# Performance work log

Hardware: AMD Instinct MI355X
Metric: run time of the kernel (lower is better)

Reference implementation:

```python
import jax, jax.numpy as jnp
import numpy as np

OMEGA_0 = 30.0  # SIREN frequency from config.kernel.omega_0


def setup_inputs() -> dict:
    key = jax.random.key(0)
    ks = jax.random.split(key, 8)
    B, Ci, Co, L, H = 8, 64, 64, 8192, 32
    x = jax.random.normal(ks[0], (B, Ci, L), dtype=jnp.float32)
    # SIREN-style kernel-net params (Linear(1,H) -> sin -> Linear(H,H) -> sin -> Linear(H, Co*Ci))
    w1 = jax.random.uniform(ks[1], (1, H), jnp.float32, -1.0, 1.0)
    b1 = jax.random.uniform(ks[2], (H,), jnp.float32, -1.0, 1.0)
    c = np.sqrt(6.0 / H) / OMEGA_0
    w2 = jax.random.uniform(ks[3], (H, H), jnp.float32, -c, c)
    b2 = jax.random.uniform(ks[4], (H,), jnp.float32, -c, c)
    w3 = jax.random.uniform(ks[5], (H, Co * Ci), jnp.float32, -c, c)
    b3 = jax.random.uniform(ks[6], (Co * Ci,), jnp.float32, -c, c)
    bias = jnp.zeros((Co,), dtype=jnp.float32)  # CKConv bias init: fill_(0.0)
    return {"x": x, "w1": w1, "b1": b1, "w2": w2, "b2": b2,
            "w3": w3, "b3": b3, "bias": bias}


def reference(x, w1, b1, w2, b2, w3, b3, bias):
    B, Ci, L = x.shape
    Co = bias.shape[0]
    # 1. relative positions in [-1, 1], one per input sample
    rel = jnp.linspace(-1.0, 1.0, L).astype(x.dtype)[:, None]        # (L, 1)
    # 2. SIREN kernel net -> continuous kernel sampled at L positions
    h = jnp.sin(OMEGA_0 * (rel @ w1 + b1))                            # (L, H)
    h = jnp.sin(OMEGA_0 * (h @ w2 + b2))                              # (L, H)
    k = (h @ w3 + b3)                                                 # (L, Co*Ci)
    kernel = k.T.reshape(Co, Ci, L)                                   # (Co, Ci, L)
    # 3. causal full-length conv1d. torch's causal_padding (left zero-pad of
    #    x by K-1, plus a left zero on an even-length kernel) + conv1d
    #    (cross-correlation) is mathematically y[t] = sum_{tau<=t} x[t-tau] *
    #    kernel_flipped[tau], i.e. a causal linear convolution with the
    #    time-reversed kernel. Computed exactly via zero-padded FFT (N=2L >=
    #    L+L-1, so no circular wraparound) instead of O(L^2) direct conv.
    kr = kernel[:, :, ::-1]                                           # flip time axis
    N = 2 * L
    Xf = jnp.fft.rfft(x, n=N, axis=-1)                                # (B, Ci, N/2+1)
    Kf = jnp.fft.rfft(kr, n=N, axis=-1)                               # (Co, Ci, N/2+1)
    Yf = jnp.einsum('bif,oif->bof', Xf, Kf)                           # contract in-channels
    y = jnp.fft.irfft(Yf, n=N, axis=-1)[:, :, :L]                     # (B, Co, L)
    return y + bias[None, :, None]
```

## Files before the change

### kernel.cpp

```cpp
#include <hip/hip_runtime.h>


#define LSEQ   8192
#define N2     8192
#define HDIM   32
#define NB     33
#define NROWS  512
#define NFREQ  8193
#define FSTRIDE 8200
#define FBLK   8
#define OMEGA0 30.0f
#define TWOPI  6.283185307179586f

#define IDX(i) ((i) + ((i) >> 4))

__global__ __launch_bounds__(256) void prep_basis_kernel(
    const float* __restrict__ w1, const float* __restrict__ b1,
    const float* __restrict__ w2, const float* __restrict__ b2,
    float* __restrict__ hbT)
{
    int t = blockIdx.x * 256 + threadIdx.x;
    float rel = -1.0f + 2.0f * (float)t / (float)(LSEQ - 1);
    float h1[HDIM];
    #pragma unroll
    for (int j = 0; j < HDIM; ++j)
        h1[j] = sinf(OMEGA0 * fmaf(rel, w1[j], b1[j]));
    for (int j = 0; j < HDIM; ++j) {
        float acc = b2[j];
        #pragma unroll 8
        for (int j2 = 0; j2 < HDIM; ++j2)
            acc = fmaf(h1[j2], w2[j2 * HDIM + j], acc);
        hbT[j * LSEQ + (LSEQ - 1 - t)] = sinf(OMEGA0 * acc);
    }
    hbT[HDIM * LSEQ + t] = 1.0f;
}

__global__ __launch_bounds__(256) void prep_m2_kernel(
    const float* __restrict__ w3, const float* __restrict__ b3,
    float* __restrict__ M2)
{
    int idx = blockIdx.x * 256 + threadIdx.x;
    if (idx >= NB * 64 * 64) return;
    int o = idx & 63;
    int i = (idx >> 6) & 63;
    int r = idx >> 12;
    M2[idx] = (r < HDIM) ? w3[r * 4096 + o * 64 + i] : b3[o * 64 + i];
}

__device__ __forceinline__ float2 tw8k(const float2* Tq, int t)
{
    bool mir = t > 1024;
    int u = mir ? 2048 - t : t;
    float2 e = Tq[u];
    float c = mir ? e.y : e.x;
    float s = mir ? e.x : e.y;
    return make_float2(c, -s);
}

__device__ __forceinline__ void build_table(float2* Tq, int tid)
{
    for (int t = tid; t <= 1024; t += 256) {
        float s, c;
        __sincosf(TWOPI * (float)t / 8192.0f, &s, &c);
        Tq[t] = make_float2(c, s);
    }
}

__device__ __forceinline__ void fft8192_core(float* re, float* im,
                                             const float2* Tq, int tid)
{
    for (int p = 11; p >= 1; p -= 2) {
        int m = 1 << p;
        int lmul = 11 - p;
        __syncthreads();
        for (int u = tid; u < 2048; u += 256) {
            int j = u & (m - 1);
            int base = ((u >> p) << (p + 2)) + j;
            int i0 = IDX(base), i1 = IDX(base + m), i2 = IDX(base + 2 * m), i3 = IDX(base + 3 * m);
            float ar = re[i0], ai = im[i0];
            float br = re[i1], bi = im[i1];
            float cr = re[i2], ci = im[i2];
            float dr = re[i3], di = im[i3];
            float t0r = ar + cr, t0i = ai + ci;
            float t1r = ar - cr, t1i = ai - ci;
            float t2r = br + dr, t2i = bi + di;
            float t3r = br - dr, t3i = bi - di;
            float q0r = t0r + t2r, q0i = t0i + t2i;
            float q2r = t0r - t2r, q2i = t0i - t2i;
            float q1r = t1r + t3i, q1i = t1i - t3r;
            float q3r = t1r - t3i, q3i = t1i + t3r;
            float2 w1 = tw8k(Tq, j << lmul);
            float w2r = w1.x * w1.x - w1.y * w1.y;
            float w2i = 2.0f * w1.x * w1.y;
            float w3r = w2r * w1.x - w2i * w1.y;
            float w3i = w2r * w1.y + w2i * w1.x;
            re[i0] = q0r;                     im[i0] = q0i;
            re[i1] = q2r * w2r - q2i * w2i;   im[i1] = q2r * w2i + q2i * w2r;
            re[i2] = q1r * w1.x - q1i * w1.y; im[i2] = q1r * w1.y + q1i * w1.x;
            re[i3] = q3r * w3r - q3i * w3i;   im[i3] = q3r * w3i + q3i * w3r;
        }
    }
    __syncthreads();
    for (int u = tid; u < 4096; u += 256) {
        int a = IDX(2 * u), b = IDX(2 * u + 1);
        float ar = re[a], ai = im[a];
        float br = re[b], bi = im[b];
        re[a] = ar + br; im[a] = ai + bi;
        re[b] = ar - br; im[b] = ai - bi;
    }
    __syncthreads();
    for (int idx = tid; idx < N2; idx += 256) {
        unsigned r = __brev((unsigned)idx) >> 19;
        if ((int)r > idx) {
            int pa = IDX(idx), pb = IDX((int)r);
            float tr = re[pa], ti = im[pa];
            re[pa] = re[pb]; im[pa] = im[pb];
            re[pb] = tr;     im[pb] = ti;
        }
    }
    __syncthreads();
}

__global__ __launch_bounds__(256) void rfft_rows_kernel(
    const float* __restrict__ in, float* __restrict__ outF)
{
    __shared__ float re[8704], im[8704];
    __shared__ float2 Tq[1025];
    int tid = threadIdx.x;
    int row = blockIdx.x;

    build_table(Tq, tid);

    const float2* zin = (const float2*)(in + (long long)row * LSEQ);
    for (int n = tid; n < 4096; n += 256) {
        float2 v = zin[n];
        re[IDX(n)] = v.x;            im[IDX(n)] = v.y;
        re[IDX(n + 4096)] = 0.0f;    im[IDX(n + 4096)] = 0.0f;
    }
    fft8192_core(re, im, Tq, tid);

    float2* out = (float2*)outF + (long long)row * FSTRIDE;
    for (int k = tid; k <= 8192; k += 256) {
        int k1 = IDX(k & (N2 - 1));
        int k2 = IDX((N2 - k) & (N2 - 1));
        float zr = re[k1], zi = im[k1];
        float wr = re[k2], wi = im[k2];
        float er = 0.5f * (zr + wr), ei = 0.5f * (zi - wi);
        float pr = 0.5f * (zi + wi), pi = 0.5f * (wr - zr);
        float s, c;
        __sincosf(-TWOPI * (float)k / 16384.0f, &s, &c);
        out[k] = make_float2(er + c * pr - s * pi,
                             ei + c * pi + s * pr);
    }
}

__global__ __launch_bounds__(256, 4) void contract_kernel(
    const float* __restrict__ Hf, const float* __restrict__ M2,
    float* __restrict__ XYf)
{
    __shared__ float2 Ks[FBLK][8][64];
    __shared__ __align__(16) float2 Xq[8][8][FBLK];
    int tid = threadIdx.x;
    int o = tid & 63;
    int qs = tid >> 6;
    long long f0 = (long long)blockIdx.x * FBLK;

    const float* Hblk = Hf + (size_t)blockIdx.x * (FBLK * 2);

    float2 yacc[2][FBLK];
    #pragma unroll
    for (int b = 0; b < 2; ++b)
        #pragma unroll
        for (int f = 0; f < FBLK; ++f) yacc[b][f] = make_float2(0.f, 0.f);

    int srow = tid >> 2;
    int sb = srow >> 3, sii = srow & 7;
    int sf = (tid & 3) << 1;

    for (int oct = 0; oct < 8; ++oct) {
        __syncthreads();

        const float4* xsrc = (const float4*)((const float2*)XYf
            + (long long)((sb << 6) + (oct << 3) + sii) * FSTRIDE + f0 + sf);
        float4 xstage = *xsrc;

        float2 kacc[2][FBLK];
        #pragma unroll
        for (int a = 0; a < 2; ++a)
            #pragma unroll
            for (int f = 0; f < FBLK; ++f) kacc[a][f] = make_float2(0.f, 0.f);

        const float* mp = M2 + (((oct << 3) + (qs << 1)) << 6) + o;
        #pragma unroll 3
        for (int r = 0; r < NB; ++r) {
            const float4* hp = (const float4*)(Hblk + (size_t)r * (size_t)(FSTRIDE * 2));
            float4 h0 = hp[0], h1 = hp[1], h2 = hp[2], h3 = hp[3];
            float m0 = mp[(r << 12)];
            float m1 = mp[(r << 12) + 64];
            float hr_[FBLK] = {h0.x,h0.z,h1.x,h1.z,h2.x,h2.z,h3.x,h3.z};
            float hi_[FBLK] = {h0.y,h0.w,h1.y,h1.w,h2.y,h2.w,h3.y,h3.w};
            #pragma unroll
            for (int f = 0; f < FBLK; ++f) {
                kacc[0][f].x = fmaf(m0, hr_[f], kacc[0][f].x);
                kacc[0][f].y = fmaf(m0, hi_[f], kacc[0][f].y);
                kacc[1][f].x = fmaf(m1, hr_[f], kacc[1][f].x);
                kacc[1][f].y = fmaf(m1, hi_[f], kacc[1][f].y);
            }
        }
        Xq[sb][sii][sf]     = make_float2(xstage.x, xstage.y);
        Xq[sb][sii][sf + 1] = make_float2(xstage.z, xstage.w);
        {
            int i0 = qs << 1;
            #pragma unroll
            for (int f = 0; f < FBLK; ++f) {
                Ks[f][i0][o]     = kacc[0][f];
                Ks[f][i0 + 1][o] = kacc[1][f];
            }
        }
        __syncthreads();

        #pragma unroll 2
        for (int ii = 0; ii < 8; ++ii) {
            const float4* xap = (const float4*)(&Xq[qs][ii][0]);
            const float4* xbp = (const float4*)(&Xq[qs + 4][ii][0]);
            float4 xa0 = xap[0], xa1 = xap[1], xa2 = xap[2], xa3 = xap[3];
            float4 xb0 = xbp[0], xb1 = xbp[1], xb2 = xbp[2], xb3 = xbp[3];
            float xar[FBLK] = {xa0.x,xa0.z,xa1.x,xa1.z,xa2.x,xa2.z,xa3.x,xa3.z};
            float xai[FBLK] = {xa0.y,xa0.w,xa1.y,xa1.w,xa2.y,xa2.w,xa3.y,xa3.w};
            float xbr[FBLK] = {xb0.x,xb0.z,xb1.x,xb1.z,xb2.x,xb2.z,xb3.x,xb3.z};
            float xbi[FBLK] = {xb0.y,xb0.w,xb1.y,xb1.w,xb2.y,xb2.w,xb3.y,xb3.w};
            #pragma unroll
            for (int f = 0; f < FBLK; ++f) {
                float2 kv = Ks[f][ii][o];
                yacc[0][f].x = fmaf(xar[f], kv.x, fmaf(-xai[f], kv.y, yacc[0][f].x));
                yacc[0][f].y = fmaf(xar[f], kv.y, fmaf( xai[f], kv.x, yacc[0][f].y));
                yacc[1][f].x = fmaf(xbr[f], kv.x, fmaf(-xbi[f], kv.y, yacc[1][f].x));
                yacc[1][f].y = fmaf(xbr[f], kv.y, fmaf( xbi[f], kv.x, yacc[1][f].y));
            }
        }
    }
    __syncthreads();

    #pragma unroll
    for (int bh = 0; bh < 2; ++bh) {
        long long row = (long long)(((qs + (bh << 2)) << 6) + o);
        float2* yp = (float2*)XYf + row * FSTRIDE + f0;
        #pragma unroll
        for (int f = 0; f < FBLK; ++f)
            if (f0 + f < NFREQ) yp[f] = yacc[bh][f];
    }
}

__global__ __launch_bounds__(256) void irfft_rows_kernel(
    const float* __restrict__ Yf, const float* __restrict__ bias,
    float* __restrict__ out)
{
    __shared__ float re[8704], im[8704];
    __shared__ float2 Tq[1025];
    int tid = threadIdx.x;
    int row = blockIdx.x;
    int o = row & 63;

    build_table(Tq, tid);

    const float2* G = (const float2*)Yf + (long long)row * FSTRIDE;
    for (int k = tid; k < N2; k += 256) {
        float2 gk = G[k];
        float2 gm = G[8192 - k];
        float er = 0.5f * (gk.x + gm.x), ei = 0.5f * (gk.y - gm.y);
        float pr = 0.5f * (gk.x - gm.x), pi = 0.5f * (gk.y + gm.y);
        float s, c;
        __sincosf(TWOPI * (float)k / 16384.0f, &s, &c);
        float or_ = pr * c - pi * s;
        float oi_ = pr * s + pi * c;
        re[IDX(k)] = er - oi_;
        im[IDX(k)] = -(ei + or_);
    }
    fft8192_core(re, im, Tq, tid);

    float bo = bias[o];
    const float scale = 1.0f / 8192.0f;
    float2* op = (float2*)(out + (long long)row * LSEQ);
    for (int n = tid; n < 4096; n += 256) {
        int pn = IDX(n);
        op[n] = make_float2(fmaf(re[pn], scale, bo), fmaf(-im[pn], scale, bo));
    }
}

extern "C" void kernel_launch(void* const* d_in, const int* in_sizes, int n_in,
                              void* d_out, int out_size, void* d_ws, size_t ws_size,
                              hipStream_t stream)
{
    const float* x    = (const float*)d_in[0];
    const float* w1   = (const float*)d_in[1];
    const float* b1   = (const float*)d_in[2];
    const float* w2   = (const float*)d_in[3];
    const float* b2   = (const float*)d_in[4];
    const float* w3   = (const float*)d_in[5];
    const float* b3   = (const float*)d_in[6];
    const float* bias = (const float*)d_in[7];
    float* out = (float*)d_out;

    float* ws  = (float*)d_ws;
    float* hbT = ws;
    float* Hf  = hbT + NB * LSEQ;
    float* M2  = Hf + NB * FSTRIDE * 2;
    float* XYf = M2 + NB * 64 * 64;

    prep_basis_kernel<<<dim3(LSEQ / 256), dim3(256), 0, stream>>>(w1, b1, w2, b2, hbT);
    prep_m2_kernel<<<dim3((NB * 64 * 64 + 255) / 256), dim3(256), 0, stream>>>(w3, b3, M2);
    rfft_rows_kernel<<<dim3(NB), dim3(256), 0, stream>>>(hbT, Hf);
    rfft_rows_kernel<<<dim3(NROWS), dim3(256), 0, stream>>>(x, XYf);
    contract_kernel<<<dim3((NFREQ + FBLK - 1) / FBLK), dim3(256), 0, stream>>>(Hf, M2, XYf);
    irfft_rows_kernel<<<dim3(NROWS), dim3(256), 0, stream>>>(XYf, bias, out);
}
```

Measured before the change: 266.3 us.

## Widen FFT blocks to 1024 threads and remap contraction to 512 threads

The FFT row kernels now run with 1024 threads per block instead of 256, so each thread does a quarter of the butterfly, bit-reversal and I/O work per stage. The contraction kernel moves to 512 threads, where each thread handles one in-channel slice and one batch instead of two of each. That halves per-thread registers and accumulators and is meant to raise occupancy and latency hiding. In exchange, each thread recomputes its kernel spectrum from the basis with less reuse per thread, and the larger FFT blocks pay more for their barriers.

New measurement: 258.6 us. -2.9%, faster.

```diff
diff --git a/kernel.cpp b/kernel.cpp
--- a/kernel.cpp
+++ b/kernel.cpp
@@ -9,6 +9,7 @@
 #define NFREQ  8193
 #define FSTRIDE 8200
 #define FBLK   8
+#define FTH    1024
 #define OMEGA0 30.0f
 #define TWOPI  6.283185307179586f
 
@@ -59,7 +60,7 @@
 
 __device__ __forceinline__ void build_table(float2* Tq, int tid)
 {
-    for (int t = tid; t <= 1024; t += 256) {
+    for (int t = tid; t <= 1024; t += FTH) {
         float s, c;
         __sincosf(TWOPI * (float)t / 8192.0f, &s, &c);
         Tq[t] = make_float2(c, s);
@@ -73,7 +74,7 @@
         int m = 1 << p;
         int lmul = 11 - p;
         __syncthreads();
-        for (int u = tid; u < 2048; u += 256) {
+        for (int u = tid; u < 2048; u += FTH) {
             int j = u & (m - 1);
             int base = ((u >> p) << (p + 2)) + j;
             int i0 = IDX(base), i1 = IDX(base + m), i2 = IDX(base + 2 * m), i3 = IDX(base + 3 * m);
@@ -101,7 +102,7 @@
         }
     }
     __syncthreads();
-    for (int u = tid; u < 4096; u += 256) {
+    for (int u = tid; u < 4096; u += FTH) {
         int a = IDX(2 * u), b = IDX(2 * u + 1);
         float ar = re[a], ai = im[a];
         float br = re[b], bi = im[b];
@@ -109,7 +110,7 @@
         re[b] = ar - br; im[b] = ai - bi;
     }
     __syncthreads();
-    for (int idx = tid; idx < N2; idx += 256) {
+    for (int idx = tid; idx < N2; idx += FTH) {
         unsigned r = __brev((unsigned)idx) >> 19;
         if ((int)r > idx) {
             int pa = IDX(idx), pb = IDX((int)r);
@@ -121,7 +122,7 @@
     __syncthreads();
 }
 
-__global__ __launch_bounds__(256) void rfft_rows_kernel(
+__global__ __launch_bounds__(FTH) void rfft_rows_kernel(
     const float* __restrict__ in, float* __restrict__ outF)
 {
     __shared__ float re[8704], im[8704];
@@ -132,7 +133,7 @@
     build_table(Tq, tid);
 
     const float2* zin = (const float2*)(in + (long long)row * LSEQ);
-    for (int n = tid; n < 4096; n += 256) {
+    for (int n = tid; n < 4096; n += FTH) {
         float2 v = zin[n];
         re[IDX(n)] = v.x;            im[IDX(n)] = v.y;
         re[IDX(n + 4096)] = 0.0f;    im[IDX(n + 4096)] = 0.0f;
@@ -140,7 +141,7 @@
     fft8192_core(re, im, Tq, tid);
 
     float2* out = (float2*)outF + (long long)row * FSTRIDE;
-    for (int k = tid; k <= 8192; k += 256) {
+    for (int k = tid; k <= 8192; k += FTH) {
         int k1 = IDX(k & (N2 - 1));
         int k2 = IDX((N2 - k) & (N2 - 1));
         float zr = re[k1], zi = im[k1];
@@ -154,7 +155,7 @@
     }
 }
 
-__global__ __launch_bounds__(256, 4) void contract_kernel(
+__global__ __launch_bounds__(512, 8) void contract_kernel(
     const float* __restrict__ Hf, const float* __restrict__ M2,
     float* __restrict__ XYf)
 {
@@ -162,96 +163,74 @@
     __shared__ __align__(16) float2 Xq[8][8][FBLK];
     int tid = threadIdx.x;
     int o = tid & 63;
-    int qs = tid >> 6;
+    int w = tid >> 6;
     long long f0 = (long long)blockIdx.x * FBLK;
 
     const float* Hblk = Hf + (size_t)blockIdx.x * (FBLK * 2);
 
-    float2 yacc[2][FBLK];
+    float2 yacc[FBLK];
     #pragma unroll
-    for (int b = 0; b < 2; ++b)
-        #pragma unroll
-        for (int f = 0; f < FBLK; ++f) yacc[b][f] = make_float2(0.f, 0.f);
-
-    int srow = tid >> 2;
-    int sb = srow >> 3, sii = srow & 7;
-    int sf = (tid & 3) << 1;
+    for (int f = 0; f < FBLK; ++f) yacc[f] = make_float2(0.f, 0.f);
+
+    int sf  = tid & 7;
+    int sii = (tid >> 3) & 7;
+    int sb  = tid >> 6;
 
     for (int oct = 0; oct < 8; ++oct) {
         __syncthreads();
 
-        const float4* xsrc = (const float4*)((const float2*)XYf
-            + (long long)((sb << 6) + (oct << 3) + sii) * FSTRIDE + f0 + sf);
-        float4 xstage = *xsrc;
-
-        float2 kacc[2][FBLK];
+        const float2* xsrc = (const float2*)XYf
+            + (long long)((sb << 6) + (oct << 3) + sii) * FSTRIDE + f0 + sf;
+        float2 xstage = *xsrc;
+
+        float2 kacc[FBLK];
         #pragma unroll
-        for (int a = 0; a < 2; ++a)
-            #pragma unroll
-            for (int f = 0; f < FBLK; ++f) kacc[a][f] = make_float2(0.f, 0.f);
-
-        const float* mp = M2 + (((oct << 3) + (qs << 1)) << 6) + o;
+        for (int f = 0; f < FBLK; ++f) kacc[f] = make_float2(0.f, 0.f);
+
+        const float* mp = M2 + (((oct << 3) + w) << 6) + o;
         #pragma unroll 3
         for (int r = 0; r < NB; ++r) {
             const float4* hp = (const float4*)(Hblk + (size_t)r * (size_t)(FSTRIDE * 2));
             float4 h0 = hp[0], h1 = hp[1], h2 = hp[2], h3 = hp[3];
-            float m0 = mp[(r << 12)];
-            float m1 = mp[(r << 12) + 64];
+            float m0 = mp[r << 12];
             float hr_[FBLK] = {h0.x,h0.z,h1.x,h1.z,h2.x,h2.z,h3.x,h3.z};
             float hi_[FBLK] = {h0.y,h0.w,h1.y,h1.w,h2.y,h2.w,h3.y,h3.w};
             #pragma unroll
             for (int f = 0; f < FBLK; ++f) {
-                kacc[0][f].x = fmaf(m0, hr_[f], kacc[0][f].x);
-                kacc[0][f].y = fmaf(m0, hi_[f], kacc[0][f].y);
-                kacc[1][f].x = fmaf(m1, hr_[f], kacc[1][f].x);
-                kacc[1][f].y = fmaf(m1, hi_[f], kacc[1][f].y);
+                kacc[f].x = fmaf(m0, hr_[f], kacc[f].x);
+                kacc[f].y = fmaf(m0, hi_[f], kacc[f].y);
             }
         }
-        Xq[sb][sii][sf]     = make_float2(xstage.x, xstage.y);
-        Xq[sb][sii][sf + 1] = make_float2(xstage.z, xstage.w);
-        {
-            int i0 = qs << 1;
-            #pragma unroll
-            for (int f = 0; f < FBLK; ++f) {
-                Ks[f][i0][o]     = kacc[0][f];
-                Ks[f][i0 + 1][o] = kacc[1][f];
-            }
-        }
+        Xq[sb][sii][sf] = xstage;
+        #pragma unroll
+        for (int f = 0; f < FBLK; ++f)
+            Ks[f][w][o] = kacc[f];
         __syncthreads();
 
         #pragma unroll 2
         for (int ii = 0; ii < 8; ++ii) {
-            const float4* xap = (const float4*)(&Xq[qs][ii][0]);
-            const float4* xbp = (const float4*)(&Xq[qs + 4][ii][0]);
-            float4 xa0 = xap[0], xa1 = xap[1], xa2 = xap[2], xa3 = xap[3];
-            float4 xb0 = xbp[0], xb1 = xbp[1], xb2 = xbp[2], xb3 = xbp[3];
-            float xar[FBLK] = {xa0.x,xa0.z,xa1.x,xa1.z,xa2.x,xa2.z,xa3.x,xa3.z};
-            float xai[FBLK] = {xa0.y,xa0.w,xa1.y,xa1.w,xa2.y,xa2.w,xa3.y,xa3.w};
-            float xbr[FBLK] = {xb0.x,xb0.z,xb1.x,xb1.z,xb2.x,xb2.z,xb3.x,xb3.z};
-            float xbi[FBLK] = {xb0.y,xb0.w,xb1.y,xb1.w,xb2.y,xb2.w,xb3.y,xb3.w};
+            const float4* xp = (const float4*)(&Xq[w][ii][0]);
+            float4 x0 = xp[0], x1 = xp[1], x2 = xp[2], x3 = xp[3];
+            float xr[FBLK] = {x0.x,x0.z,x1.x,x1.z,x2.x,x2.z,x3.x,x3.z};
+            float xi[FBLK] = {x0.y,x0.w,x1.y,x1.w,x2.y,x2.w,x3.y,x3.w};
             #pragma unroll
             for (int f = 0; f < FBLK; ++f) {
                 float2 kv = Ks[f][ii][o];
-                yacc[0][f].x = fmaf(xar[f], kv.x, fmaf(-xai[f], kv.y, yacc[0][f].x));
-                yacc[0][f].y = fmaf(xar[f], kv.y, fmaf( xai[f], kv.x, yacc[0][f].y));
-                yacc[1][f].x = fmaf(xbr[f], kv.x, fmaf(-xbi[f], kv.y, yacc[1][f].x));
-                yacc[1][f].y = fmaf(xbr[f], kv.y, fmaf( xbi[f], kv.x, yacc[1][f].y));
+                yacc[f].x = fmaf(xr[f], kv.x, fmaf(-xi[f], kv.y, yacc[f].x));
+                yacc[f].y = fmaf(xr[f], kv.y, fmaf( xi[f], kv.x, yacc[f].y));
             }
         }
     }
     __syncthreads();
 
+    long long row = (long long)((w << 6) + o);
+    float2* yp = (float2*)XYf + row * FSTRIDE + f0;
     #pragma unroll
-    for (int bh = 0; bh < 2; ++bh) {
-        long long row = (long long)(((qs + (bh << 2)) << 6) + o);
-        float2* yp = (float2*)XYf + row * FSTRIDE + f0;
-        #pragma unroll
-        for (int f = 0; f < FBLK; ++f)
-            if (f0 + f < NFREQ) yp[f] = yacc[bh][f];
-    }
-}
-
-__global__ __launch_bounds__(256) void irfft_rows_kernel(
+    for (int f = 0; f < FBLK; ++f)
+        if (f0 + f < NFREQ) yp[f] = yacc[f];
+}
+
+__global__ __launch_bounds__(FTH) void irfft_rows_kernel(
     const float* __restrict__ Yf, const float* __restrict__ bias,
     float* __restrict__ out)
 {
@@ -264,7 +243,7 @@
     build_table(Tq, tid);
 
     const float2* G = (const float2*)Yf + (long long)row * FSTRIDE;
-    for (int k = tid; k < N2; k += 256) {
+    for (int k = tid; k < N2; k += FTH) {
         float2 gk = G[k];
         float2 gm = G[8192 - k];
         float er = 0.5f * (gk.x + gm.x), ei = 0.5f * (gk.y - gm.y);
@@ -281,7 +260,7 @@
     float bo = bias[o];
     const float scale = 1.0f / 8192.0f;
     float2* op = (float2*)(out + (long long)row * LSEQ);
-    for (int n = tid; n < 4096; n += 256) {
+    for (int n = tid; n < 4096; n += FTH) {
         int pn = IDX(n);
         op[n] = make_float2(fmaf(re[pn], scale, bo), fmaf(-im[pn], scale, bo));
     }
@@ -309,8 +288,8 @@
 
     prep_basis_kernel<<<dim3(LSEQ / 256), dim3(256), 0, stream>>>(w1, b1, w2, b2, hbT);
     prep_m2_kernel<<<dim3((NB * 64 * 64 + 255) / 256), dim3(256), 0, stream>>>(w3, b3, M2);
-    rfft_rows_kernel<<<dim3(NB), dim3(256), 0, stream>>>(hbT, Hf);
-    rfft_rows_kernel<<<dim3(NROWS), dim3(256), 0, stream>>>(x, XYf);
-    contract_kernel<<<dim3((NFREQ + FBLK - 1) / FBLK), dim3(256), 0, stream>>>(Hf, M2, XYf);
-    irfft_rows_kernel<<<dim3(NROWS), dim3(256), 0, stream>>>(XYf, bias, out);
-}
+    rfft_rows_kernel<<<dim3(NB), dim3(FTH), 0, stream>>>(hbT, Hf);
+    rfft_rows_kernel<<<dim3(NROWS), dim3(FTH), 0, stream>>>(x, XYf);
+    contract_kernel<<<dim3((NFREQ + FBLK - 1) / FBLK), dim3(512), 0, stream>>>(Hf, M2, XYf);
+    irfft_rows_kernel<<<dim3(NROWS), dim3(FTH), 0, stream>>>(XYf, bias, out);
+}
```
